# Optimization experiments

Measured on AMD Instinct MI355X. Metric: run time of the kernel, lower is better.

## Reference

```python
import jax, jax.numpy as jnp
import numpy as np

N = 20000      # nodes
E = 320000     # edges (avg degree 16)
DIN, H1, H2, DOUT = 256, 256, 128, 64


def _lin_params(key, din, dout):
    kw, kb = jax.random.split(key)
    s = 1.0 / np.sqrt(din)
    W = jax.random.uniform(kw, (din, dout), jnp.float32, -s, s)
    b = jax.random.uniform(kb, (dout,), jnp.float32, -s, s)
    return W, b


def setup_inputs() -> dict:
    key = jax.random.key(0)
    keys = jax.random.split(key, 20)
    inp = {
        'x': jax.random.normal(keys[0], (N, DIN), jnp.float32),
        'edge_index': jax.random.randint(keys[1], (2, E), 0, N, jnp.int64),
    }
    dims = [(DIN, H1), (DIN, H1), (DIN, H1),   # layer1 key/query/value
            (H1, H2), (H1, H2), (H1, H2),      # layer2
            (H2, DOUT), (H2, DOUT), (H2, DOUT)]  # layer3
    names = ['k1', 'q1', 'v1', 'k2', 'q2', 'v2', 'k3', 'q3', 'v3']
    for i, (nm, (di, do)) in enumerate(zip(names, dims)):
        W, b = _lin_params(keys[2 + i], di, do)
        inp[nm + '_w'] = W
        inp[nm + '_b'] = b
    # skip (root) weights, no bias per PyG, plus per-conv output bias
    for j, (di, do) in enumerate([(DIN, H1), (H1, H2), (H2, DOUT)], start=1):
        s = 1.0 / np.sqrt(di)
        inp[f's{j}_w'] = jax.random.uniform(keys[11 + 2 * j], (di, do), jnp.float32, -s, s)
        inp[f'bias{j}'] = jnp.zeros((do,), jnp.float32)
    return inp


def _res_gated_conv(x, src, dst, kw, kb, qw, qb, vw, vb, sw, bias):
    # PyG ResGatedGraphConv (flow source_to_target, aggr='add', act=Sigmoid):
    # out_i = lin_skip(x_i) + sum_{j->i} sigmoid(lin_key(x_i) + lin_query(x_j)) * lin_value(x_j) + bias
    k = x @ kw + kb            # [N, D]
    q = x @ qw + qb
    v = x @ vw + vb
    eta = jax.nn.sigmoid(k[dst] + q[src])   # [E, D] edge gate
    msg = eta * v[src]                      # [E, D]
    agg = jax.ops.segment_sum(msg, dst, num_segments=N)  # scatter-add to targets
    return x @ sw + agg + bias


def reference(x, edge_index,
              k1_w, k1_b, q1_w, q1_b, v1_w, v1_b,
              k2_w, k2_b, q2_w, q2_b, v2_w, v2_b,
              k3_w, k3_b, q3_w, q3_b, v3_w, v3_b,
              s1_w, bias1, s2_w, bias2, s3_w, bias3):
    src, dst = edge_index[0], edge_index[1]
    h = _res_gated_conv(x, src, dst, k1_w, k1_b, q1_w, q1_b, v1_w, v1_b, s1_w, bias1)
    # dropout (eval mode -> identity)
    h = _res_gated_conv(h, src, dst, k2_w, k2_b, q2_w, q2_b, v2_w, v2_b, s2_w, bias2)
    h = _res_gated_conv(h, src, dst, k3_w, k3_b, q3_w, q3_b, v3_w, v3_b, s3_w, bias3)
    return jax.nn.softmax(h, axis=1)
```

## Files before the change

### kernel.cpp

```cpp
#include <hip/hip_runtime.h>
#include <hip/hip_bf16.h>
#include <type_traits>


#define NN 20000
#define EE 320000
#define ELLW 64

typedef _Float16 half8 __attribute__((ext_vector_type(8)));
typedef _Float16 half4 __attribute__((ext_vector_type(4)));
typedef _Float16 half2v __attribute__((ext_vector_type(2)));
typedef float f32x4 __attribute__((ext_vector_type(4)));

__device__ __forceinline__ _Float16 f2h(float f) { return (_Float16)f; }
__device__ __forceinline__ float fsigmoid_mul(float v, float x) {
    return v * __builtin_amdgcn_rcpf(1.f + __expf(-x));
}

struct PrepArgs {
    const float* w[3][4];
    const float* b[3][4];
    _Float16* wt[3];
    float* cb[3];
};

__global__ __launch_bounds__(256) void setup_all_kernel(
    const int* __restrict__ ei, int* __restrict__ deg, int* __restrict__ flag,
    const float* __restrict__ x, _Float16* __restrict__ Xh, PrepArgs a) {
    const int b = blockIdx.x;
    const int tid = threadIdx.x;
    if (b < 79) {
        const int i = b * 256 + tid;
        if (i < NN) deg[i] = 0;
    } else if (b == 79) {
        __shared__ int nz;
        if (tid == 0) nz = 0;
        __syncthreads();
        int c = 0;
        for (int t = tid; t < 1024; t += 256)
            if (ei[2 * t + 1] != 0) c = 1;
        if (c) atomicAdd(&nz, 1);
        __syncthreads();
        if (tid == 0) *flag = (nz == 0) ? 1 : 0;
    } else if (b < 1744) {
        const int idx = (b - 80) * 256 + tid;
        int layer, li, K, D;
        if (idx < 262144) {
            layer = 0; li = idx; K = 256; D = 256;
        } else if (idx < 393216) {
            layer = 1; li = idx - 262144; K = 256; D = 128;
        } else {
            layer = 2; li = idx - 393216; K = 128; D = 64;
        }
        const int p = li / K;
        const int k = li - p * K;
        int grp, dim;
        if (layer < 2) {
            const int c = p >> 7;
            const int local = p & 127;
            if (local < 32) {
                grp = 0; dim = c * 32 + local;
            } else if (local < 96) {
                const int t = local - 32;
                const int g8 = t >> 3, r = t & 7;
                grp = (r < 4) ? 1 : 2;
                dim = c * 32 + g8 * 4 + (r & 3);
            } else {
                grp = 3; dim = c * 32 + local - 96;
            }
        } else {
            if (p < 64) {
                grp = 0; dim = p;
            } else if (p < 192) {
                const int t = p - 64;
                grp = (t & 1) ? 2 : 1;
                dim = t >> 1;
            } else {
                grp = 3; dim = p - 192;
            }
        }
        a.wt[layer][(size_t)p * K + k] =
            f2h(a.w[layer][grp][(size_t)k * D + dim]);
        if (k == 0) a.cb[layer][p] = a.b[layer][grp][dim];
    } else {
        const int i = ((b - 1744) * 256 + tid) * 8;
        if (i < NN * 256) {
            const float4 f0 = *(const float4*)(x + i);
            const float4 f1 = *(const float4*)(x + i + 4);
            half8 h;
            h[0] = f2h(f0.x); h[1] = f2h(f0.y); h[2] = f2h(f0.z); h[3] = f2h(f0.w);
            h[4] = f2h(f1.x); h[5] = f2h(f1.y); h[6] = f2h(f1.z); h[7] = f2h(f1.w);
            *(half8*)(Xh + i) = h;
        }
    }
}

template <bool CHUNKED>
__device__ __forceinline__ void gemm_tile(
    int bm, int bn, const _Float16* __restrict__ A,
    const _Float16* __restrict__ Bt, const float* __restrict__ catbias,
    _Float16* __restrict__ O, int M, int K, int N) {
    __shared__ _Float16 As[2][4096];
    __shared__ _Float16 Bs[2][4096];

    const int tid = threadIdx.x;
    const int wid = tid >> 6;
    const int lane = tid & 63;
    const int tile_m = bm * 128;
    const int tile_n = bn * 128;
    const int wm = (wid & 1) * 64;
    const int wn = (wid >> 1) * 64;

    const int st_row = (wid << 4) + (lane >> 2);
    const int st_kc = (lane & 3) << 3;

    auto stage = [&](int buf, int kt) {
#pragma unroll
        for (int j = 0; j < 2; ++j) {
            int ar = tile_m + j * 64 + st_row;
            ar = ar < M ? ar : M - 1;
            const _Float16* ag = A + (size_t)ar * K + kt + st_kc;
            __builtin_amdgcn_global_load_lds(
                (const __attribute__((address_space(1))) unsigned int*)ag,
                (__attribute__((address_space(3))) unsigned int*)
                    &As[buf][j * 2048 + (wid << 9)],
                16, 0, 0);
            const int br = tile_n + j * 64 + st_row;
            const _Float16* bg = Bt + (size_t)br * K + kt + st_kc;
            __builtin_amdgcn_global_load_lds(
                (const __attribute__((address_space(1))) unsigned int*)bg,
                (__attribute__((address_space(3))) unsigned int*)
                    &Bs[buf][j * 2048 + (wid << 9)],
                16, 0, 0);
        }
    };

    stage(0, 0);

    f32x4 acc[4][4] = {};
    const int fr = lane & 15;
    const int fk = (lane >> 4) << 3;
    const int niter = K >> 5;

    for (int it = 0; it < niter; ++it) {
        __syncthreads();
        if (it + 1 < niter) stage((it + 1) & 1, (it + 1) << 5);
        const _Float16* as = As[it & 1];
        const _Float16* bs = Bs[it & 1];
        half8 af[4], bf[4];
#pragma unroll
        for (int mi = 0; mi < 4; ++mi)
            af[mi] = *(const half8*)&as[(wm + mi * 16 + fr) * 32 + fk];
#pragma unroll
        for (int ni = 0; ni < 4; ++ni)
            bf[ni] = *(const half8*)&bs[(wn + ni * 16 + fr) * 32 + fk];
#pragma unroll
        for (int mi = 0; mi < 4; ++mi)
#pragma unroll
            for (int ni = 0; ni < 4; ++ni)
                acc[mi][ni] = __builtin_amdgcn_mfma_f32_16x16x32_f16(
                    af[mi], bf[ni], acc[mi][ni], 0, 0, 0);
    }
    __syncthreads();

    _Float16* zone = &As[0][0] + wid * 2048;
    const int cl = lane & 15;
    const int rq = (lane >> 4) << 2;
    const int col0 = tile_n + wn;
    const int r0 = tile_m + wm;

    _Float16* obase;
    int ostride;
    if constexpr (CHUNKED) {
        obase = O + (size_t)(col0 >> 7) * NN * 128 + (col0 & 127);
        ostride = 128;
    } else {
        obase = O + col0;
        ostride = N;
    }
#pragma unroll
    for (int mi = 0; mi < 4; ++mi) {
#pragma unroll
        for (int ni = 0; ni < 4; ++ni) {
            const float cb = catbias[col0 + ni * 16 + cl];
#pragma unroll
            for (int r = 0; r < 4; ++r)
                zone[(rq + r) * 72 + ni * 16 + cl] = f2h(acc[mi][ni][r] + cb);
        }
#pragma unroll
        for (int j = 0; j < 2; ++j) {
            const int rr = j * 8 + (lane >> 3);
            const int row = r0 + mi * 16 + rr;
            const half8 v = *(const half8*)&zone[rr * 72 + (lane & 7) * 8];
            if (row < M)
                *(half8*)&obase[(size_t)row * ostride + (lane & 7) * 8] = v;
        }
    }
}

template <bool CHUNKED>
__global__ __launch_bounds__(256) void gemm_kernel(
    const _Float16* __restrict__ A, const _Float16* __restrict__ Bt,
    const float* __restrict__ catbias, _Float16* __restrict__ O, int M, int K,
    int N, int mblocks) {
    gemm_tile<CHUNKED>(blockIdx.x % mblocks, blockIdx.x / mblocks, A, Bt,
                       catbias, O, M, K, N);
}

__global__ __launch_bounds__(256) void gemm1_fill_kernel(
    const _Float16* __restrict__ A, const _Float16* __restrict__ Bt,
    const float* __restrict__ catbias, _Float16* __restrict__ O,
    const int* __restrict__ ei, const int* __restrict__ i64flag,
    int* __restrict__ deg, unsigned short* __restrict__ col) {
    if (blockIdx.x < 1256) {
        gemm_tile<true>(blockIdx.x % 157, blockIdx.x / 157, A, Bt, catbias, O,
                        NN, 256, 1024);
        return;
    }
    const int e = (blockIdx.x - 1256) * 256 + threadIdx.x;
    if (e >= EE) return;
    int src, dst;
    if (*i64flag) {
        const long long* p = (const long long*)ei;
        src = (int)p[e];
        dst = (int)p[EE + e];
    } else {
        src = ei[e];
        dst = ei[EE + e];
    }
    const int pos = atomicAdd(&deg[dst], 1);
    if (pos < ELLW) col[dst * ELLW + pos] = (unsigned short)src;
}

template <int NCH>
__global__ __launch_bounds__(256) void gather_chunked_kernel(
    const int* __restrict__ deg, const unsigned short* __restrict__ col,
    const _Float16* __restrict__ KQVS, _Float16* __restrict__ Hh, int n) {
    const int b = blockIdx.x;
    int chunk, group;
    if constexpr (NCH == 8) {
        chunk = b & 7;
        group = b >> 3;
    } else {
        const int slot = b & 7;
        chunk = slot & 3;
        group = ((b >> 3) << 1) | (slot >> 2);
    }
    const int wid = threadIdx.x >> 6;
    const int node = group * 4 + wid;
    if (node >= n) return;
    const int lane = threadIdx.x & 63;
    const int j = lane & 7;
    const int g = lane >> 3;

    const _Float16* cbase = KQVS + (size_t)chunk * NN * 128;
    const _Float16* nb = cbase + (size_t)node * 128;

    int dg = deg[node];
    dg = dg < ELLW ? dg : ELLW;
    int idx = (int)col[node * ELLW + lane];
    if (lane >= dg) idx = node;

    float k[4], acc[4] = {0.f, 0.f, 0.f, 0.f};
    {
        const half4 u = *(const half4*)(nb + j * 4);
#pragma unroll
        for (int t = 0; t < 4; ++t) k[t] = (float)u[t];
    }

    auto qvacc = [&](half8 u) {
#pragma unroll
        for (int t = 0; t < 4; ++t)
            acc[t] += fsigmoid_mul((float)u[4 + t], k[t] + (float)u[t]);
    };
    auto qvload = [&](int e) {
        const int s = __shfl(idx, e, 64);
        return *(const half8*)(cbase + (size_t)s * 128 + 32 + j * 8);
    };

    const int R = (dg + 7) >> 3;
    int e = g;
    half8 u = qvload(e);
    for (int i = 1; i < R; ++i) {
        const int en = i * 8 + g;
        const half8 un = qvload(en);
        if (e < dg) qvacc(u);
        u = un;
        e = en;
    }
    if (R > 0 && e < dg) qvacc(u);

#pragma unroll
    for (int t = 0; t < 4; ++t) {
        acc[t] += __shfl_xor(acc[t], 8, 64);
        acc[t] += __shfl_xor(acc[t], 16, 64);
        acc[t] += __shfl_xor(acc[t], 32, 64);
    }

    if (g == 0) {
        const half4 s4 = *(const half4*)(nb + 96 + j * 4);
        half4 o;
#pragma unroll
        for (int t = 0; t < 4; ++t) o[t] = f2h((float)s4[t] + acc[t]);
        *(half4*)(Hh + (size_t)node * (NCH * 32) + chunk * 32 + j * 4) = o;
    }
}

__global__ __launch_bounds__(256) void edge_gather3_kernel(
    const int* __restrict__ deg, const unsigned short* __restrict__ col,
    const _Float16* __restrict__ KQVS, float* __restrict__ out, int n) {
    const int node = blockIdx.x * 4 + (threadIdx.x >> 6);
    if (node >= n) return;
    const int lane = threadIdx.x & 63;

    int dg = deg[node];
    dg = dg < ELLW ? dg : ELLW;
    int idx = (int)col[node * ELLW + lane];
    if (lane >= dg) idx = node;

    const float k = (float)KQVS[(size_t)node * 256 + lane];
    float acc = 0.f;
    const _Float16* qvbase = KQVS + 64 + 2 * lane;

    for (int e = 0; e < dg; e += 8) {
        half2v u[8];
#pragma unroll
        for (int t = 0; t < 8; ++t) {
            const int s = __shfl(idx, e + t, 64);
            u[t] = *(const half2v*)(qvbase + (size_t)s * 256);
        }
        const int nb = dg - e;
#pragma unroll
        for (int t = 0; t < 8; ++t)
            if (t < nb) acc += fsigmoid_mul((float)u[t][1], k + (float)u[t][0]);
    }

    const float h = (float)KQVS[(size_t)node * 256 + 192 + lane] + acc;

    float m = h;
#pragma unroll
    for (int off = 32; off > 0; off >>= 1)
        m = fmaxf(m, __shfl_xor(m, off, 64));
    const float ex = __expf(h - m);
    float sm = ex;
#pragma unroll
    for (int off = 32; off > 0; off >>= 1) sm += __shfl_xor(sm, off, 64);
    out[(size_t)node * 64 + lane] = ex * __builtin_amdgcn_rcpf(sm);
}

extern "C" void kernel_launch(void* const* d_in, const int* in_sizes, int n_in,
                              void* d_out, int out_size, void* d_ws,
                              size_t ws_size, hipStream_t stream) {
    const float* x = (const float*)d_in[0];
    const int* ei = (const int*)d_in[1];

    char* w = (char*)d_ws;
    _Float16* Xh = (_Float16*)w;     w += (size_t)NN * 256 * 2;
    _Float16* KQVS = (_Float16*)w;   w += (size_t)NN * 1024 * 2;
    _Float16* H1h = (_Float16*)w;    w += (size_t)NN * 256 * 2;
    _Float16* H2h = (_Float16*)w;    w += (size_t)NN * 128 * 2;
    _Float16* Wt1 = (_Float16*)w;    w += (size_t)1024 * 256 * 2;
    _Float16* Wt2 = (_Float16*)w;    w += (size_t)512 * 256 * 2;
    _Float16* Wt3 = (_Float16*)w;    w += (size_t)256 * 128 * 2;
    float* cb1 = (float*)w;          w += 1024 * 4;
    float* cb2 = (float*)w;          w += 512 * 4;
    float* cb3 = (float*)w;          w += 256 * 4;
    int* i64flag = (int*)w;          w += 16;
    int* deg = (int*)w;              w += (size_t)NN * 4;
    unsigned short* ell = (unsigned short*)w;  w += (size_t)NN * ELLW * 2;

    const dim3 blk(256);

    PrepArgs pa;
    pa.w[0][0] = (const float*)d_in[2];  pa.b[0][0] = (const float*)d_in[3];
    pa.w[0][1] = (const float*)d_in[4];  pa.b[0][1] = (const float*)d_in[5];
    pa.w[0][2] = (const float*)d_in[6];  pa.b[0][2] = (const float*)d_in[7];
    pa.w[1][0] = (const float*)d_in[8];  pa.b[1][0] = (const float*)d_in[9];
    pa.w[1][1] = (const float*)d_in[10]; pa.b[1][1] = (const float*)d_in[11];
    pa.w[1][2] = (const float*)d_in[12]; pa.b[1][2] = (const float*)d_in[13];
    pa.w[2][0] = (const float*)d_in[14]; pa.b[2][0] = (const float*)d_in[15];
    pa.w[2][1] = (const float*)d_in[16]; pa.b[2][1] = (const float*)d_in[17];
    pa.w[2][2] = (const float*)d_in[18]; pa.b[2][2] = (const float*)d_in[19];
    pa.w[0][3] = (const float*)d_in[20]; pa.b[0][3] = (const float*)d_in[21];
    pa.w[1][3] = (const float*)d_in[22]; pa.b[1][3] = (const float*)d_in[23];
    pa.w[2][3] = (const float*)d_in[24]; pa.b[2][3] = (const float*)d_in[25];
    pa.wt[0] = Wt1; pa.wt[1] = Wt2; pa.wt[2] = Wt3;
    pa.cb[0] = cb1; pa.cb[1] = cb2; pa.cb[2] = cb3;

    setup_all_kernel<<<4244, blk, 0, stream>>>(ei, deg, i64flag, x, Xh, pa);

    gemm1_fill_kernel<<<2506, blk, 0, stream>>>(Xh, Wt1, cb1, KQVS, ei,
                                                i64flag, deg, ell);
    gather_chunked_kernel<8><<<40000, blk, 0, stream>>>(deg, ell, KQVS, H1h,
                                                        NN);

    gemm_kernel<true><<<157 * 4, blk, 0, stream>>>(H1h, Wt2, cb2, KQVS, NN,
                                                   256, 512, 157);
    gather_chunked_kernel<4><<<20000, blk, 0, stream>>>(deg, ell, KQVS, H2h,
                                                        NN);

    gemm_kernel<false><<<157 * 2, blk, 0, stream>>>(H2h, Wt3, cb3, KQVS, NN,
                                                    128, 256, 157);
    edge_gather3_kernel<<<(NN + 3) / 4, blk, 0, stream>>>(deg, ell, KQVS,
                                                          (float*)d_out, NN);
}
```

Measured before the change: 272.2 us.

## Pad ELL with a zero sentinel row to drop per-edge bounds checks in gathers

Pre-fills the ELL neighbour table with the index NN and adds a zeroed sentinel row at index NN in each KQVS chunk. Padding slots then read zeros and contribute nothing, so the gather kernels can drop their per-edge degree masks. The chunked gather now issues all neighbour loads up front into an 8-entry register array before computing, replacing the software-pipelined loop, and the gate uses exp2 with a prescaled key fused into FMAs. The cost is a larger setup kernel that initialises the whole ELL table, a bigger KQVS buffer, and more registers per thread for the load batch.

```diff
diff --git a/kernel.cpp b/kernel.cpp
--- a/kernel.cpp
+++ b/kernel.cpp
@@ -6,6 +6,7 @@
 #define NN 20000
 #define EE 320000
 #define ELLW 64
+#define NL2E -1.4426950408889634f
 
 typedef _Float16 half8 __attribute__((ext_vector_type(8)));
 typedef _Float16 half4 __attribute__((ext_vector_type(4)));
@@ -13,8 +14,10 @@
 typedef float f32x4 __attribute__((ext_vector_type(4)));
 
 __device__ __forceinline__ _Float16 f2h(float f) { return (_Float16)f; }
-__device__ __forceinline__ float fsigmoid_mul(float v, float x) {
-    return v * __builtin_amdgcn_rcpf(1.f + __expf(-x));
+__device__ __forceinline__ float gate_acc(float acc, float qf, float vf,
+                                          float kpre) {
+    const float e = __builtin_amdgcn_exp2f(fmaf(qf, NL2E, kpre));
+    return fmaf(vf, __builtin_amdgcn_rcpf(1.f + e), acc);
 }
 
 struct PrepArgs {
@@ -26,7 +29,9 @@
 
 __global__ __launch_bounds__(256) void setup_all_kernel(
     const int* __restrict__ ei, int* __restrict__ deg, int* __restrict__ flag,
-    const float* __restrict__ x, _Float16* __restrict__ Xh, PrepArgs a) {
+    const float* __restrict__ x, _Float16* __restrict__ Xh,
+    unsigned int* __restrict__ ell_i, unsigned int* __restrict__ kqvs_i,
+    PrepArgs a) {
     const int b = blockIdx.x;
     const int tid = threadIdx.x;
     if (b < 79) {
@@ -82,7 +87,7 @@
         a.wt[layer][(size_t)p * K + k] =
             f2h(a.w[layer][grp][(size_t)k * D + dim]);
         if (k == 0) a.cb[layer][p] = a.b[layer][grp][dim];
-    } else {
+    } else if (b < 4244) {
         const int i = ((b - 1744) * 256 + tid) * 8;
         if (i < NN * 256) {
             const float4 f0 = *(const float4*)(x + i);
@@ -91,6 +96,15 @@
             h[0] = f2h(f0.x); h[1] = f2h(f0.y); h[2] = f2h(f0.z); h[3] = f2h(f0.w);
             h[4] = f2h(f1.x); h[5] = f2h(f1.y); h[6] = f2h(f1.z); h[7] = f2h(f1.w);
             *(half8*)(Xh + i) = h;
+        }
+    } else if (b < 6744) {
+        const int i = (b - 4244) * 256 + tid;
+        if (i < NN * ELLW / 2) ell_i[i] = 0x4E204E20u;
+    } else {
+        for (int i = tid; i < 512; i += 256) {
+            const int c = i >> 6;
+            const int off = i & 63;
+            kqvs_i[((size_t)c * (NN + 1) + NN) * 64 + off] = 0u;
         }
     }
 }
@@ -172,7 +186,7 @@
     _Float16* obase;
     int ostride;
     if constexpr (CHUNKED) {
-        obase = O + (size_t)(col0 >> 7) * NN * 128 + (col0 & 127);
+        obase = O + (size_t)(col0 >> 7) * (NN + 1) * 128 + (col0 & 127);
         ostride = 128;
     } else {
         obase = O + col0;
@@ -203,6 +217,12 @@
     const _Float16* __restrict__ A, const _Float16* __restrict__ Bt,
     const float* __restrict__ catbias, _Float16* __restrict__ O, int M, int K,
     int N, int mblocks) {
+    if constexpr (!CHUNKED) {
+        if (blockIdx.x == 0 && threadIdx.x < 64) {
+            half4 z = {};
+            *(half4*)&O[(size_t)NN * N + threadIdx.x * 4] = z;
+        }
+    }
     gemm_tile<CHUNKED>(blockIdx.x % mblocks, blockIdx.x / mblocks, A, Bt,
                        catbias, O, M, K, N);
 }
@@ -253,42 +273,36 @@
     const int j = lane & 7;
     const int g = lane >> 3;
 
-    const _Float16* cbase = KQVS + (size_t)chunk * NN * 128;
+    const _Float16* cbase = KQVS + (size_t)chunk * (NN + 1) * 128;
     const _Float16* nb = cbase + (size_t)node * 128;
 
     int dg = deg[node];
     dg = dg < ELLW ? dg : ELLW;
-    int idx = (int)col[node * ELLW + lane];
-    if (lane >= dg) idx = node;
-
-    float k[4], acc[4] = {0.f, 0.f, 0.f, 0.f};
+    const int R = (__builtin_amdgcn_readfirstlane(dg) + 7) >> 3;
+    const int idx = (int)col[node * ELLW + lane];
+
+    float kpre[4], acc[4] = {0.f, 0.f, 0.f, 0.f};
     {
         const half4 u = *(const half4*)(nb + j * 4);
 #pragma unroll
-        for (int t = 0; t < 4; ++t) k[t] = (float)u[t];
-    }
-
-    auto qvacc = [&](half8 u) {
-#pragma unroll
-        for (int t = 0; t < 4; ++t)
-            acc[t] += fsigmoid_mul((float)u[4 + t], k[t] + (float)u[t]);
-    };
-    auto qvload = [&](int e) {
-        const int s = __shfl(idx, e, 64);
-        return *(const half8*)(cbase + (size_t)s * 128 + 32 + j * 8);
-    };
-
-    const int R = (dg + 7) >> 3;
-    int e = g;
-    half8 u = qvload(e);
-    for (int i = 1; i < R; ++i) {
-        const int en = i * 8 + g;
-        const half8 un = qvload(en);
-        if (e < dg) qvacc(u);
-        u = un;
-        e = en;
-    }
-    if (R > 0 && e < dg) qvacc(u);
+        for (int t = 0; t < 4; ++t) kpre[t] = (float)u[t] * NL2E;
+    }
+
+    half8 u[8];
+#pragma unroll
+    for (int i = 0; i < 8; ++i)
+        if (i < R) {
+            const int s = __shfl(idx, i * 8 + g, 64);
+            u[i] = *(const half8*)(cbase + (size_t)s * 128 + 32 + j * 8);
+        }
+#pragma unroll
+    for (int i = 0; i < 8; ++i)
+        if (i < R) {
+#pragma unroll
+            for (int t = 0; t < 4; ++t)
+                acc[t] = gate_acc(acc[t], (float)u[i][t], (float)u[i][4 + t],
+                                  kpre[t]);
+        }
 
 #pragma unroll
     for (int t = 0; t < 4; ++t) {
@@ -315,24 +329,23 @@
 
     int dg = deg[node];
     dg = dg < ELLW ? dg : ELLW;
-    int idx = (int)col[node * ELLW + lane];
-    if (lane >= dg) idx = node;
-
-    const float k = (float)KQVS[(size_t)node * 256 + lane];
+    const int R = (__builtin_amdgcn_readfirstlane(dg) + 7) >> 3;
+    const int idx = (int)col[node * ELLW + lane];
+
+    const float kpre = (float)KQVS[(size_t)node * 256 + lane] * NL2E;
     float acc = 0.f;
     const _Float16* qvbase = KQVS + 64 + 2 * lane;
 
-    for (int e = 0; e < dg; e += 8) {
+    for (int i = 0; i < R; ++i) {
         half2v u[8];
 #pragma unroll
         for (int t = 0; t < 8; ++t) {
-            const int s = __shfl(idx, e + t, 64);
+            const int s = __shfl(idx, i * 8 + t, 64);
             u[t] = *(const half2v*)(qvbase + (size_t)s * 256);
         }
-        const int nb = dg - e;
 #pragma unroll
         for (int t = 0; t < 8; ++t)
-            if (t < nb) acc += fsigmoid_mul((float)u[t][1], k + (float)u[t][0]);
+            acc = gate_acc(acc, (float)u[t][0], (float)u[t][1], kpre);
     }
 
     const float h = (float)KQVS[(size_t)node * 256 + 192 + lane] + acc;
@@ -356,7 +369,7 @@
 
     char* w = (char*)d_ws;
     _Float16* Xh = (_Float16*)w;     w += (size_t)NN * 256 * 2;
-    _Float16* KQVS = (_Float16*)w;   w += (size_t)NN * 1024 * 2;
+    _Float16* KQVS = (_Float16*)w;   w += (size_t)8 * (NN + 1) * 128 * 2;
     _Float16* H1h = (_Float16*)w;    w += (size_t)NN * 256 * 2;
     _Float16* H2h = (_Float16*)w;    w += (size_t)NN * 128 * 2;
     _Float16* Wt1 = (_Float16*)w;    w += (size_t)1024 * 256 * 2;
@@ -387,7 +400,8 @@
     pa.wt[0] = Wt1; pa.wt[1] = Wt2; pa.wt[2] = Wt3;
     pa.cb[0] = cb1; pa.cb[1] = cb2; pa.cb[2] = cb3;
 
-    setup_all_kernel<<<4244, blk, 0, stream>>>(ei, deg, i64flag, x, Xh, pa);
+    setup_all_kernel<<<6745, blk, 0, stream>>>(
+        ei, deg, i64flag, x, Xh, (unsigned int*)ell, (unsigned int*)KQVS, pa);
 
     gemm1_fill_kernel<<<2506, blk, 0, stream>>>(Xh, Wt1, cb1, KQVS, ei,
                                                 i64flag, deg, ell);
```

Result: no change. 274.6 us (+0.9%).
